# Kernel optimization log

Hardware: AMD Instinct MI355X
Metric: run time of the kernel (lower is better)

Reference implementation:

```python
import jax, jax.numpy as jnp
import numpy as np
import math

N, S, E, H = 4, 4096, 1024, 16
D = E // H  # head_dim = 64


def setup_inputs() -> dict:
    key = jax.random.key(0)
    ks = jax.random.split(key, 9)
    w = 1.0 / math.sqrt(E)
    mk = lambda k, shape: (jax.random.normal(k, shape, jnp.float32) * w)
    return {
        "x": jax.random.normal(ks[0], (N, S, E), jnp.float32),
        "Wq": mk(ks[1], (E, E)), "bq": mk(ks[2], (E,)),
        "Wk": mk(ks[3], (E, E)), "bk": mk(ks[4], (E,)),
        "Wv": mk(ks[5], (E, E)), "bv": mk(ks[6], (E,)),
        "Wo": mk(ks[7], (E, E)), "bo": mk(ks[8], (E,)),
    }


def reference(x, Wq, bq, Wk, bk, Wv, bv, Wo, bo):
    n, s, e = x.shape
    h, d = H, D
    scale = 1.0 / math.sqrt(d)

    def proj(W, b):
        # nn.Linear: x @ W.T + b, then view(N,S,H,D).transpose(1,2) -> (N,H,S,D)
        y = jnp.einsum('nse,fe->nsf', x, W) + b
        return y.reshape(n, s, h, d).transpose(0, 2, 1, 3)  # (N,H,S,D)

    Q = proj(Wq, bq)
    K = proj(Wk, bk)
    V = proj(Wv, bv)

    # Faithful reproduction of the source's einsum applied to ALREADY-transposed
    # (N,H,S,D) tensors: labels n,q,h,d bind to actual dims N,H,S,D, so the
    # result is (N, S, H, H) -- heads attending to heads at each position.
    scores = jnp.einsum('nqhd,nkhd->nhqk', Q, K) * scale  # (N,S,H,H)
    attn = jax.nn.softmax(scores, axis=-1)
    # Second einsum: attn labels n,h,q,l bind to N,S,H,H; V labels n,l,h,d bind
    # to N,H,S,D. Output nqhd has actual shape (N,H,S,D).
    out = jnp.einsum('nhql,nlhd->nqhd', attn, V)  # (N,H,S,D)
    out = out.reshape(n, s, e)  # scrambled flat reshape, as in the source
    return jnp.einsum('nse,fe->nsf', out, Wo) + bo
```

## Files before the change

kernel.cpp:

```cpp
#include <hip/hip_runtime.h>
#include <hip/hip_fp16.h>
#include <stddef.h>
#include <stdint.h>


typedef _Float16 f16_t;
typedef _Float16 f16x8 __attribute__((ext_vector_type(8)));
typedef _Float16 f16x4 __attribute__((ext_vector_type(4)));
typedef float    f32x4 __attribute__((ext_vector_type(4)));

static constexpr int Sdim = 4096;
static constexpr int Edim = 1024;
static constexpr int Mrows = 4 * Sdim;
static constexpr size_t MATEL = (size_t)Mrows * Edim;
static constexpr size_t WEL = (size_t)Edim * Edim;

__device__ __forceinline__ void gload_lds16(const f16_t* g, f16_t* l) {
  __builtin_amdgcn_global_load_lds(
      (const __attribute__((address_space(1))) void*)g,
      (__attribute__((address_space(3))) void*)l, 16, 0, 0);
}

__device__ __forceinline__ f16x8 ds_read16(uint32_t byte_addr) {
  f16x8 r;
  asm volatile("ds_read_b128 %0, %1" : "=v"(r) : "v"(byte_addr));
  return r;
}

#define SCHED_FENCE() __builtin_amdgcn_sched_barrier(0)

__global__ __launch_bounds__(256) void cvt_kernel(
    const float* __restrict__ s0, const float* __restrict__ s1,
    const float* __restrict__ s2, const float* __restrict__ s3,
    const float* __restrict__ s4,
    f16_t* __restrict__ d0, f16_t* __restrict__ d1, f16_t* __restrict__ d2,
    f16_t* __restrict__ d3, f16_t* __restrict__ d4) {
  const float* s; f16_t* d; size_t nv;
  switch (blockIdx.y) {
    case 0: s = s0; d = d0; nv = MATEL / 4; break;
    case 1: s = s1; d = d1; nv = WEL / 4; break;
    case 2: s = s2; d = d2; nv = WEL / 4; break;
    case 3: s = s3; d = d3; nv = WEL / 4; break;
    default: s = s4; d = d4; nv = WEL / 4; break;
  }
  const size_t stride = (size_t)gridDim.x * 256;
  for (size_t i = blockIdx.x * 256 + threadIdx.x; i < nv; i += stride) {
    const f32x4 v = ((const f32x4*)s)[i];
    f16x4 h;
#pragma unroll
    for (int j = 0; j < 4; j++) h[j] = (f16_t)v[j];
    ((f16x4*)d)[i] = h;
  }
}

static constexpr int BM2 = 256, BN2 = 256, BK2 = 64;
static constexpr int NT2 = Edim / BK2;
static constexpr int HALF2 = 128 * BK2;

template <int V> struct ic { static constexpr int v = V; };

template <typename TOut>
__device__ __forceinline__ void gemm256(const f16_t* __restrict__ A,
                                        const f16_t* __restrict__ B,
                                        const float* __restrict__ bias,
                                        TOut* __restrict__ C) {
  __shared__ __align__(16) f16_t lds[2][2][2][HALF2];

  const int t = threadIdx.x;
  const int lane = t & 63;
  const int w = t >> 6;
  const int l16 = lane & 15;
  const int quad = lane >> 4;
  const int ha = w >> 2;
  const int hb = (w & 3) >> 1;
  const int wnr = (w & 1) * 64;

  const uint32_t ldsBase = (uint32_t)(uintptr_t)
      (__attribute__((address_space(3))) f16_t*)&lds[0][0][0][0];
  const uint32_t aHalfOff = (uint32_t)(ha * (HALF2 * 2));
  const uint32_t bHalfOff = (uint32_t)(32768 + hb * (HALF2 * 2));

  const int id = blockIdx.x;
  const int id2 = (id & 7) * 32 + (id >> 3);
  const int bm = (id2 & 63) * BM2;
  const int bn = (id2 >> 6) * BN2;

  const int srow = w * 8 + (lane >> 3);
  const int scol = ((lane & 7) ^ ((lane >> 3) & 7)) * 8;
  const size_t gA0 = (size_t)(bm + srow) * Edim + scol;
  const size_t gB0 = (size_t)(bn + srow) * Edim + scol;
  const int lws = w * 512 + lane * 8;

  auto stage = [&](int mat, int half, int slot, int kt) {
    const f16_t* g = (mat == 0 ? A + gA0 : B + gB0) +
                     (size_t)half * 128 * Edim + kt * BK2;
    f16_t* l = &lds[slot][mat][half][lws];
    gload_lds16(g, l);
    gload_lds16(g + (size_t)64 * Edim, l + 4096);
  };

  auto rdaddr = [&](uint32_t base, int r, int c0) -> uint32_t {
    return base + (uint32_t)((r * 64 + (c0 ^ ((r & 7) << 3))) * 2);
  };

  f32x4 acc[8][4] = {};
  f16x8 af0[4], af1[4], bf0[4], bf1[4];

  auto rdA = [&](uint32_t aBase, int ih, int kc, f16x8* dst) {
#pragma unroll
    for (int ii = 0; ii < 4; ++ii) {
      const int r = ih * 64 + ii * 16 + l16;
      dst[ii] = ds_read16(rdaddr(aBase, r, kc * 32 + quad * 8));
    }
  };
  auto rdB = [&](uint32_t bBase, int kc, f16x8* dst) {
#pragma unroll
    for (int j = 0; j < 4; ++j) {
      const int r = wnr + j * 16 + l16;
      dst[j] = ds_read16(rdaddr(bBase, r, kc * 32 + quad * 8));
    }
  };
  auto mmac = [&](const f16x8* af, const f16x8* bf, int ih) {
    __builtin_amdgcn_s_setprio(1);
#pragma unroll
    for (int ii = 0; ii < 4; ++ii)
#pragma unroll
      for (int j = 0; j < 4; ++j)
        acc[ih * 4 + ii][j] = __builtin_amdgcn_mfma_f32_16x16x32_f16(
            af[ii], bf[j], acc[ih * 4 + ii][j], 0, 0, 0);
    __builtin_amdgcn_s_setprio(0);
  };

  stage(0, 0, 0, 0); stage(0, 1, 0, 0);
  stage(1, 0, 0, 0); stage(1, 1, 0, 0);
  stage(1, 0, 1, 1); stage(1, 1, 1, 1);
  asm volatile("s_waitcnt vmcnt(2)");
  SCHED_FENCE();
  __builtin_amdgcn_s_barrier();
  SCHED_FENCE();
  rdA(ldsBase + aHalfOff, 0, 0, af0);
  rdB(ldsBase + bHalfOff, 0, bf0);

  auto ktile = [&](int tt, auto SAc, auto SBc, auto NQc) {
    constexpr int SA = decltype(SAc)::v;
    constexpr int SB = decltype(SBc)::v;
    constexpr int NQ = decltype(NQc)::v;
    const int S = tt & 1;
    const uint32_t aB  = ldsBase + (uint32_t)(S * 65536) + aHalfOff;
    const uint32_t bB  = ldsBase + (uint32_t)(S * 65536) + bHalfOff;
    const uint32_t aBn = ldsBase + (uint32_t)((S ^ 1) * 65536) + aHalfOff;
    const uint32_t bBn = ldsBase + (uint32_t)((S ^ 1) * 65536) + bHalfOff;
    rdA(aB, 1, 0, af1);
    if (SA) { stage(0, 0, S ^ 1, tt + 1); stage(0, 1, S ^ 1, tt + 1); }
    SCHED_FENCE();
    asm volatile("s_waitcnt lgkmcnt(4)");
    SCHED_FENCE();
    mmac(af0, bf0, 0);
    rdA(aB, 0, 1, af0);
    rdB(bB, 1, bf1);
    SCHED_FENCE();
    asm volatile("s_waitcnt lgkmcnt(8)");
    SCHED_FENCE();
    mmac(af1, bf0, 1);
    rdA(aB, 1, 1, af1);
    SCHED_FENCE();
    asm volatile("s_waitcnt lgkmcnt(4)");
    SCHED_FENCE();
    mmac(af0, bf1, 0);
    asm volatile("s_waitcnt lgkmcnt(0)");
    asm volatile("s_waitcnt vmcnt(0)");
    SCHED_FENCE();
    __builtin_amdgcn_s_barrier();
    SCHED_FENCE();
    if (SB) { stage(1, 0, S, tt + 2); stage(1, 1, S, tt + 2); }
    if (NQ) { rdA(aBn, 0, 0, af0); rdB(bBn, 0, bf0); }
    SCHED_FENCE();
    mmac(af1, bf1, 1);
  };

  for (int tt = 0; tt < NT2 - 2; ++tt) ktile(tt, ic<1>{}, ic<1>{}, ic<1>{});
  ktile(NT2 - 2, ic<1>{}, ic<0>{}, ic<1>{});
  ktile(NT2 - 1, ic<0>{}, ic<0>{}, ic<0>{});

  const int wm = ha * 128;
  const int wn = (w & 3) * 64;
#pragma unroll
  for (int j = 0; j < 4; ++j) {
    const int col = bn + wn + j * 16 + l16;
    const float bv = bias[col];
#pragma unroll
    for (int i = 0; i < 8; ++i) {
      const int rb = bm + wm + i * 16 + quad * 4;
#pragma unroll
      for (int r = 0; r < 4; ++r)
        C[(size_t)(rb + r) * Edim + col] = (TOut)(acc[i][j][r] + bv);
    }
  }
}

__global__ __launch_bounds__(512, 1) void qkv_kernel(
    const f16_t* __restrict__ x,
    const f16_t* __restrict__ Wq, const float* __restrict__ bq,
    const f16_t* __restrict__ Wk, const float* __restrict__ bk,
    const f16_t* __restrict__ Wv, const float* __restrict__ bv,
    f16_t* __restrict__ Qb, f16_t* __restrict__ Kb, f16_t* __restrict__ Vb) {
  const f16_t* W; const float* bi; f16_t* C;
  if (blockIdx.z == 0)      { W = Wq; bi = bq; C = Qb; }
  else if (blockIdx.z == 1) { W = Wk; bi = bk; C = Kb; }
  else                      { W = Wv; bi = bv; C = Vb; }
  gemm256<f16_t>(x, W, bi, C);
}

__global__ __launch_bounds__(512, 1) void outp_kernel(
    const f16_t* __restrict__ Ab, const f16_t* __restrict__ Wo,
    const float* __restrict__ bo, float* __restrict__ out) {
  gemm256<float>(Ab, Wo, bo, out);
}

__global__ __launch_bounds__(256) void attn_kernel(const f16_t* __restrict__ Qb,
                                                   const f16_t* __restrict__ Kb,
                                                   const f16_t* __restrict__ Vb,
                                                   f16_t* __restrict__ Ab) {
  __shared__ __align__(16) f16_t Vs[4][1024];
  const int t = threadIdx.x;
  const int w = t >> 6;
  const int lane = t & 63;
  const int l16 = lane & 15;
  const int quad = lane >> 4;
  const int pos = blockIdx.x * 4 + w;
  const int n4 = pos >> 12;
  const int s = pos & (Sdim - 1);

  const f16_t* Qr = Qb + (size_t)pos * Edim;
  const f16_t* Kr = Kb + (size_t)pos * Edim;
  const f16_t* Vr = Vb + (size_t)pos * Edim;

  *(f16x8*)&Vs[w][lane * 16]     = *(const f16x8*)(Vr + lane * 16);
  *(f16x8*)&Vs[w][lane * 16 + 8] = *(const f16x8*)(Vr + lane * 16 + 8);

  f32x4 sacc = {};
#pragma unroll
  for (int step = 0; step < 2; step++) {
    const int off = l16 * 64 + step * 32 + quad * 8;
    const f16x8 kf = *(const f16x8*)(Kr + off);
    const f16x8 qf = *(const f16x8*)(Qr + off);
    sacc = __builtin_amdgcn_mfma_f32_16x16x32_f16(kf, qf, sacc, 0, 0, 0);
  }
#pragma unroll
  for (int r = 0; r < 4; r++) sacc[r] *= 0.125f;

  float m = fmaxf(fmaxf(sacc[0], sacc[1]), fmaxf(sacc[2], sacc[3]));
  m = fmaxf(m, __shfl_xor(m, 16));
  m = fmaxf(m, __shfl_xor(m, 32));
  float e[4];
#pragma unroll
  for (int r = 0; r < 4; r++) e[r] = __expf(sacc[r] - m);
  float l = (e[0] + e[1]) + (e[2] + e[3]);
  l += __shfl_xor(l, 16);
  l += __shfl_xor(l, 32);
  const float inv = 1.0f / l;
  f16x4 pa;
#pragma unroll
  for (int r = 0; r < 4; r++) pa[r] = (f16_t)(e[r] * inv);

  __syncthreads();
  f32x4 oacc[4];
#pragma unroll
  for (int dc = 0; dc < 4; dc++) {
    f16x4 vbf;
#pragma unroll
    for (int j = 0; j < 4; j++)
      vbf[j] = Vs[w][(quad * 4 + j) * 64 + dc * 16 + l16];
    f32x4 z = {};
    oacc[dc] = __builtin_amdgcn_mfma_f32_16x16x16f16(pa, vbf, z, 0, 0, 0);
  }

  const size_t obase =
      ((size_t)(n4 << 12) + (size_t)(s >> 4)) * Edim + (size_t)(s & 15) * 64 + l16;
#pragma unroll
  for (int reg = 0; reg < 4; reg++) {
    const size_t rowoff = obase + (size_t)(quad * 4 + reg) * 256 * Edim;
#pragma unroll
    for (int dc = 0; dc < 4; dc++)
      Ab[rowoff + dc * 16] = (f16_t)oacc[dc][reg];
  }
}

extern "C" void kernel_launch(void* const* d_in, const int* in_sizes, int n_in,
                              void* d_out, int out_size, void* d_ws, size_t ws_size,
                              hipStream_t stream) {
  const float* x  = (const float*)d_in[0];
  const float* Wq = (const float*)d_in[1];
  const float* bq = (const float*)d_in[2];
  const float* Wk = (const float*)d_in[3];
  const float* bk = (const float*)d_in[4];
  const float* Wv = (const float*)d_in[5];
  const float* bv = (const float*)d_in[6];
  const float* Wo = (const float*)d_in[7];
  const float* bo = (const float*)d_in[8];
  float* out = (float*)d_out;

  f16_t* xh  = (f16_t*)d_ws;
  f16_t* Wqh = xh + MATEL;
  f16_t* Wkh = Wqh + WEL;
  f16_t* Wvh = Wkh + WEL;
  f16_t* Woh = Wvh + WEL;
  f16_t* Qb  = Woh + WEL;
  f16_t* Kb  = Qb + MATEL;
  f16_t* Vb  = Kb + MATEL;
  f16_t* Ab  = Vb + MATEL;

  cvt_kernel<<<dim3(2048, 5), dim3(256), 0, stream>>>(x, Wq, Wk, Wv, Wo,
                                                      xh, Wqh, Wkh, Wvh, Woh);
  const int ngrid = (Mrows / BM2) * (Edim / BN2);
  qkv_kernel<<<dim3(ngrid, 1, 3), dim3(512), 0, stream>>>(
      xh, Wqh, bq, Wkh, bk, Wvh, bv, Qb, Kb, Vb);
  attn_kernel<<<dim3(Mrows / 4), dim3(256), 0, stream>>>(Qb, Kb, Vb, Ab);
  outp_kernel<<<dim3(ngrid), dim3(512), 0, stream>>>(Ab, Woh, bo, out);
}
```

Measured before the change: 339.6 us.

## Fuse Q/K/V projections into one GEMM kernel sharing the X tile

Replaces the three separate 256x256-tile projection GEMMs with a single kernel that loads each 128x64 X tile once and multiplies it against the matching Wq, Wk and Wv tiles. The aim is to cut repeated global and LDS traffic for X by a factor of three. In exchange it uses smaller tiles (128x64 per weight) with 2 blocks per CU and a simpler double buffer with a barrier every k-step, so arithmetic intensity per weight tile is lower and register pressure is high from 24 accumulator fragments.

```diff
diff --git a/kernel.cpp b/kernel.cpp
--- a/kernel.cpp
+++ b/kernel.cpp
@@ -53,6 +53,117 @@
   }
 }
 
+static constexpr int FBM = 128, FBN = 64, FBK = 64;
+static constexpr int FNT = Edim / FBK;
+
+__global__ __launch_bounds__(256, 2) void qkv_fused_kernel(
+    const f16_t* __restrict__ Xh,
+    const f16_t* __restrict__ Wq, const f16_t* __restrict__ Wk,
+    const f16_t* __restrict__ Wv,
+    const float* __restrict__ bq, const float* __restrict__ bk,
+    const float* __restrict__ bv,
+    f16_t* __restrict__ Qb, f16_t* __restrict__ Kb, f16_t* __restrict__ Vb) {
+  __shared__ __align__(16) f16_t As[2][FBM * FBK];
+  __shared__ __align__(16) f16_t Bs[2][3][FBN * FBK];
+
+  const int t = threadIdx.x;
+  const int lane = t & 63;
+  const int w = t >> 6;
+  const int l16 = lane & 15;
+  const int quad = lane >> 4;
+  const int wm = (w >> 1) * 64;
+  const int wn = (w & 1) * 32;
+
+  const int id = blockIdx.x;
+  const int id2 = (id & 7) * 256 + (id >> 3);
+  const int mt = id2 & 127;
+  const int nt = id2 >> 7;
+  const int bm = mt * FBM;
+  const int bn = nt * FBN;
+
+  const int srow = t >> 3;
+  const int scol = ((t & 7) ^ ((t >> 3) & 7)) * 8;
+  const f16_t* gA  = Xh + (size_t)(bm + srow) * Edim + scol;
+  const f16_t* gW0 = Wq + (size_t)(bn + srow) * Edim + scol;
+  const f16_t* gW1 = Wk + (size_t)(bn + srow) * Edim + scol;
+  const f16_t* gW2 = Wv + (size_t)(bn + srow) * Edim + scol;
+
+  auto stageTile = [&](int slot, int kt) {
+    const int ko = kt * FBK;
+#pragma unroll
+    for (int i = 0; i < 4; ++i)
+      gload_lds16(gA + (size_t)i * 32 * Edim + ko,
+                  &As[slot][i * 2048 + t * 8]);
+#pragma unroll
+    for (int i = 0; i < 2; ++i) {
+      gload_lds16(gW0 + (size_t)i * 32 * Edim + ko,
+                  &Bs[slot][0][i * 2048 + t * 8]);
+      gload_lds16(gW1 + (size_t)i * 32 * Edim + ko,
+                  &Bs[slot][1][i * 2048 + t * 8]);
+      gload_lds16(gW2 + (size_t)i * 32 * Edim + ko,
+                  &Bs[slot][2][i * 2048 + t * 8]);
+    }
+  };
+
+  f32x4 acc[3][4][2] = {};
+
+  stageTile(0, 0);
+  __syncthreads();
+
+  for (int kt = 0; kt < FNT; ++kt) {
+    const int S = kt & 1;
+    if (kt + 1 < FNT) stageTile(S ^ 1, kt + 1);
+
+    f16x8 af[2][4], bf[3][2][2];
+#pragma unroll
+    for (int kc = 0; kc < 2; ++kc) {
+#pragma unroll
+      for (int m = 0; m < 4; ++m) {
+        const int r = wm + m * 16 + l16;
+        af[kc][m] = *(const f16x8*)
+            &As[S][r * FBK + ((kc * 32 + quad * 8) ^ ((r & 7) << 3))];
+      }
+#pragma unroll
+      for (int c = 0; c < 3; ++c)
+#pragma unroll
+        for (int n = 0; n < 2; ++n) {
+          const int r = wn + n * 16 + l16;
+          bf[c][n][kc] = *(const f16x8*)
+              &Bs[S][c][r * FBK + ((kc * 32 + quad * 8) ^ ((r & 7) << 3))];
+        }
+    }
+#pragma unroll
+    for (int kc = 0; kc < 2; ++kc)
+#pragma unroll
+      for (int c = 0; c < 3; ++c)
+#pragma unroll
+        for (int m = 0; m < 4; ++m)
+#pragma unroll
+          for (int n = 0; n < 2; ++n)
+            acc[c][m][n] = __builtin_amdgcn_mfma_f32_16x16x32_f16(
+                af[kc][m], bf[c][n][kc], acc[c][m][n], 0, 0, 0);
+    __syncthreads();
+  }
+
+  f16_t* const outs[3] = {Qb, Kb, Vb};
+  const float* const biases[3] = {bq, bk, bv};
+#pragma unroll
+  for (int c = 0; c < 3; ++c) {
+#pragma unroll
+    for (int n = 0; n < 2; ++n) {
+      const int col = bn + wn + n * 16 + l16;
+      const float bb = biases[c][col];
+#pragma unroll
+      for (int m = 0; m < 4; ++m) {
+        const int r0 = bm + wm + m * 16 + quad * 4;
+#pragma unroll
+        for (int r = 0; r < 4; ++r)
+          outs[c][(size_t)(r0 + r) * Edim + col] = (f16_t)(acc[c][m][n][r] + bb);
+      }
+    }
+  }
+}
+
 static constexpr int BM2 = 256, BN2 = 256, BK2 = 64;
 static constexpr int NT2 = Edim / BK2;
 static constexpr int HALF2 = 128 * BK2;
@@ -196,19 +307,6 @@
         C[(size_t)(rb + r) * Edim + col] = (TOut)(acc[i][j][r] + bv);
     }
   }
-}
-
-__global__ __launch_bounds__(512, 1) void qkv_kernel(
-    const f16_t* __restrict__ x,
-    const f16_t* __restrict__ Wq, const float* __restrict__ bq,
-    const f16_t* __restrict__ Wk, const float* __restrict__ bk,
-    const f16_t* __restrict__ Wv, const float* __restrict__ bv,
-    f16_t* __restrict__ Qb, f16_t* __restrict__ Kb, f16_t* __restrict__ Vb) {
-  const f16_t* W; const float* bi; f16_t* C;
-  if (blockIdx.z == 0)      { W = Wq; bi = bq; C = Qb; }
-  else if (blockIdx.z == 1) { W = Wk; bi = bk; C = Kb; }
-  else                      { W = Wv; bi = bv; C = Vb; }
-  gemm256<f16_t>(x, W, bi, C);
 }
 
 __global__ __launch_bounds__(512, 1) void outp_kernel(
@@ -312,9 +410,9 @@
 
   cvt_kernel<<<dim3(2048, 5), dim3(256), 0, stream>>>(x, Wq, Wk, Wv, Wo,
                                                       xh, Wqh, Wkh, Wvh, Woh);
+  qkv_fused_kernel<<<dim3((Mrows / FBM) * (Edim / FBN)), dim3(256), 0, stream>>>(
+      xh, Wqh, Wkh, Wvh, bq, bk, bv, Qb, Kb, Vb);
+  attn_kernel<<<dim3(Mrows / 4), dim3(256), 0, stream>>>(Qb, Kb, Vb, Ab);
   const int ngrid = (Mrows / BM2) * (Edim / BN2);
-  qkv_kernel<<<dim3(ngrid, 1, 3), dim3(512), 0, stream>>>(
-      xh, Wqh, bq, Wkh, bk, Wvh, bv, Qb, Kb, Vb);
-  attn_kernel<<<dim3(Mrows / 4), dim3(256), 0, stream>>>(Qb, Kb, Vb, Ab);
   outp_kernel<<<dim3(ngrid), dim3(512), 0, stream>>>(Ab, Woh, bo, out);
 }
```

Measured after the change: 347.6 us. 2.3% more time.
